# Performance work log

Hardware: AMD Instinct MI355X
Metric: run time of the kernel (lower is better)

Reference implementation:

```python
import jax, jax.numpy as jnp
import numpy as np

B, L, D, H, DH, DFF, NL, A = 32, 1024, 512, 8, 64, 2048, 6, 21
CL = 4  # new variables per clique (chain junction tree)


def _build_mask():
    # Mirrors _make_junction_tree_mask: each position attends to itself,
    # to all parent-clique variables, and to earlier vars in its own clique.
    m = np.zeros((L, L), dtype=bool)
    for c in range(L // CL):
        own = range(c * CL, (c + 1) * CL)
        par = range((c - 1) * CL, c * CL) if c > 0 else range(0)
        for i in own:
            m[i, i] = True
            for p in par:
                m[i, p] = True
            for v in own:
                if v < i:
                    m[i, v] = True
    return m


def setup_inputs() -> dict:
    key = jax.random.key(0)
    ks = jax.random.split(key, 12)
    s = 0.02
    inp = {
        "x": jax.random.randint(ks[0], (B, L), 0, A, dtype=jnp.int32),
        "mask": jnp.asarray(_build_mask())[None, None],  # (1,1,L,L), broadcasts over B,H
        "tok_emb": jax.random.normal(ks[1], (A, D)) * s,
        "pos_emb": jax.random.normal(ks[2], (L, D)) * s,
        "wq": jax.random.normal(ks[3], (NL, D, D)) * s,
        "bq": jnp.zeros((NL, D)),
        "wk": jax.random.normal(ks[4], (NL, D, D)) * s,
        "bk": jnp.zeros((NL, D)),
        "wv": jax.random.normal(ks[5], (NL, D, D)) * s,
        "bv": jnp.zeros((NL, D)),
        "wo": jax.random.normal(ks[6], (NL, D, D)) * s,
        "bo": jnp.zeros((NL, D)),
        "ln1_s": jnp.ones((NL, D)),
        "ln1_b": jnp.zeros((NL, D)),
        "ln2_s": jnp.ones((NL, D)),
        "ln2_b": jnp.zeros((NL, D)),
        "w1": jax.random.normal(ks[7], (NL, D, DFF)) * s,
        "b1": jnp.zeros((NL, DFF)),
        "w2": jax.random.normal(ks[8], (NL, DFF, D)) * s,
        "b2": jnp.zeros((NL, D)),
        "wout": jax.random.normal(ks[9], (D, A)) * s,
        "bout": jnp.zeros((A,)),
    }
    return inp


def _ln(x, s, b):
    mu = x.mean(-1, keepdims=True)
    var = ((x - mu) ** 2).mean(-1, keepdims=True)
    return (x - mu) * jax.lax.rsqrt(var + 1e-6) * s + b


def reference(x, mask, tok_emb, pos_emb, wq, bq, wk, bk, wv, bv, wo, bo,
              ln1_s, ln1_b, ln2_s, ln2_b, w1, b1, w2, b2, wout, bout):
    h = tok_emb[x] + pos_emb[None, :, :]           # (B, L, D)
    neg = jnp.asarray(-1e9, h.dtype)
    scale = jnp.asarray(1.0 / np.sqrt(DH), h.dtype)
    for l in range(NL):
        # masked multi-head self-attention (pre-LN block)
        hn = _ln(h, ln1_s[l], ln1_b[l])
        q = (hn @ wq[l] + bq[l]).reshape(B, L, H, DH)
        k = (hn @ wk[l] + bk[l]).reshape(B, L, H, DH)
        v = (hn @ wv[l] + bv[l]).reshape(B, L, H, DH)
        sc = jnp.einsum('blhd,bmhd->bhlm', q, k) * scale
        sc = jnp.where(mask, sc, neg)              # junction-tree sparsity pattern
        attn = jax.nn.softmax(sc, axis=-1)
        o = jnp.einsum('bhlm,bmhd->blhd', attn, v).reshape(B, L, D) @ wo[l] + bo[l]
        h = h + o
        # feed-forward
        hn = _ln(h, ln2_s[l], ln2_b[l])
        h = h + (jax.nn.gelu(hn @ w1[l] + b1[l]) @ w2[l] + b2[l])
    return h @ wout + bout                          # (B, L, alphabet_size)
```

## Files before the change

### kernel.cpp

```cpp
#include <hip/hip_runtime.h>

#define BB 32
#define LL 1024
#define DD 512
#define HH 8
#define DHH 64
#define DFF 2048
#define NLAYERS 6
#define AA 21
#define MTOT (BB*LL)
#define QS 1536

typedef unsigned short u16;
typedef __bf16 bf16x8 __attribute__((ext_vector_type(8)));
typedef float f32x4 __attribute__((ext_vector_type(4)));
typedef u16 u16x8 __attribute__((ext_vector_type(8)));

__device__ __forceinline__ float bf2f(u16 u) {
    return __uint_as_float(((unsigned int)u) << 16);
}
__device__ __forceinline__ u16 f2bf(float f) {
    unsigned int i = __float_as_uint(f);
    unsigned int r = i + 0x7FFFu + ((i >> 16) & 1u);
    return (u16)(r >> 16);
}

__global__ void detect_kernel(const void* __restrict__ tok, int* __restrict__ flag) {
    __shared__ int cnt[256];
    int t = threadIdx.x;
    const u16* p = (const u16*)tok;
    int c = 0;
    #pragma unroll
    for (int j = 0; j < 8; j++) {
        u16 u = p[2 * (t * 8 + j)];
        int e = (u >> 7) & 0xFF;
        c += (e >= 97 && e <= 137) ? 1 : 0;
    }
    cnt[t] = c;
    __syncthreads();
    for (int s = 128; s; s >>= 1) {
        if (t < s) cnt[t] += cnt[t + s];
        __syncthreads();
    }
    if (t == 0) flag[0] = (cnt[0] > 1024) ? 1 : 0;
}

#define NTAB 13
struct ConvTab {
    const void* src[NTAB];
    unsigned long long dstOff[NTAB];
    int n[NTAB];
    int chunk[NTAB];
    int lstride[NTAB];
};
__global__ __launch_bounds__(256) void conv_small(ConvTab tab, u16* __restrict__ spBase,
                                                  const int* __restrict__ flag, int total) {
    int i = blockIdx.x * 256 + threadIdx.x;
    if (i >= total) return;
    int fl = flag[0];
    #pragma unroll 1
    for (int e = 0; e < NTAB; e++) {
        if (i < tab.n[e]) {
            const void* s = tab.src[e];
            u16 val = fl ? ((const u16*)s)[i] : f2bf(((const float*)s)[i]);
            int c = i / tab.chunk[e];
            int r = i - c * tab.chunk[e];
            spBase[tab.dstOff[e] + (size_t)c * tab.lstride[e] + r] = val;
            return;
        }
        i -= tab.n[e];
    }
}

__global__ __launch_bounds__(256) void conv_T(const void* __restrict__ src,
                                              u16* __restrict__ dst, int R, int C,
                                              const int* __restrict__ flag, int dstZS) {
    __shared__ u16 tile[32][33];
    int z = blockIdx.z;
    size_t zoffS = (size_t)z * R * C;
    size_t zoffD = (size_t)z * dstZS;
    int bx = blockIdx.x * 32, by = blockIdx.y * 32;
    int tx = threadIdx.x & 31, ty = threadIdx.x >> 5;
    int fl = flag[0];
    const u16* s16 = (const u16*)src + zoffS;
    const float* s32 = (const float*)src + zoffS;
    #pragma unroll
    for (int r = 0; r < 4; r++) {
        size_t idx = (size_t)(by + ty * 4 + r) * C + bx + tx;
        tile[ty * 4 + r][tx] = fl ? s16[idx] : f2bf(s32[idx]);
    }
    __syncthreads();
    #pragma unroll
    for (int r = 0; r < 4; r++)
        dst[zoffD + (size_t)(bx + ty * 4 + r) * R + by + tx] = tile[tx][ty * 4 + r];
}

__global__ __launch_bounds__(256) void woutpad_kernel(const void* __restrict__ wout,
                                                      const void* __restrict__ bout,
                                                      u16* __restrict__ wpad,
                                                      u16* __restrict__ bpad,
                                                      const int* __restrict__ flag) {
    int i = blockIdx.x * 256 + threadIdx.x;
    int fl = flag[0];
    if (i < 128 * 512) {
        int n = i >> 9, kk = i & 511;
        u16 val = 0;
        if (n < AA) val = fl ? ((const u16*)wout)[kk * AA + n] : f2bf(((const float*)wout)[kk * AA + n]);
        wpad[(size_t)n * 512 + kk] = val;
    }
    if (i < 128) {
        u16 val = 0;
        if (i < AA) val = fl ? ((const u16*)bout)[i] : f2bf(((const float*)bout)[i]);
        bpad[i] = val;
    }
}

__global__ __launch_bounds__(128) void embed_kernel(const int* __restrict__ x,
                                                    const u16* __restrict__ tok_emb,
                                                    const u16* __restrict__ pos_emb,
                                                    u16* __restrict__ h) {
    int row = blockIdx.x;
    int l = row & (LL - 1);
    int tok = x[row];
    int c = threadIdx.x * 4;
    ushort4 te = *(const ushort4*)(tok_emb + (size_t)tok * DD + c);
    ushort4 pe = *(const ushort4*)(pos_emb + (size_t)l * DD + c);
    ushort4 o;
    o.x = f2bf(bf2f(te.x) + bf2f(pe.x));
    o.y = f2bf(bf2f(te.y) + bf2f(pe.y));
    o.z = f2bf(bf2f(te.z) + bf2f(pe.z));
    o.w = f2bf(bf2f(te.w) + bf2f(pe.w));
    *(ushort4*)(h + (size_t)row * DD + c) = o;
}

__global__ __launch_bounds__(256) void ln_kernel(const u16* __restrict__ h,
                                                 const u16* __restrict__ s,
                                                 const u16* __restrict__ b,
                                                 u16* __restrict__ outp) {
    int row = blockIdx.x * 4 + (threadIdx.x >> 6);
    int lane = threadIdx.x & 63;
    u16x8 hv = *(const u16x8*)(h + (size_t)row * DD + lane * 8);
    float v[8];
    #pragma unroll
    for (int i = 0; i < 8; i++) v[i] = bf2f(hv[i]);
    float sum = v[0]+v[1]+v[2]+v[3]+v[4]+v[5]+v[6]+v[7];
    #pragma unroll
    for (int off = 32; off; off >>= 1) sum += __shfl_xor(sum, off, 64);
    float mu = sum * (1.0f / DD);
    float var = 0.f;
    #pragma unroll
    for (int i = 0; i < 8; i++) {
        float d = v[i] - mu;
        var += d * d;
    }
    #pragma unroll
    for (int off = 32; off; off >>= 1) var += __shfl_xor(var, off, 64);
    float rs = rsqrtf(var * (1.0f / DD) + 1e-6f);
    u16x8 sv = *(const u16x8*)(s + lane * 8);
    u16x8 bv = *(const u16x8*)(b + lane * 8);
    u16x8 o;
    #pragma unroll
    for (int i = 0; i < 8; i++)
        o[i] = f2bf((v[i] - mu) * rs * bf2f(sv[i]) + bf2f(bv[i]));
    *(u16x8*)(outp + (size_t)row * DD + lane * 8) = o;
}

#define GLD16(gp, lp) __builtin_amdgcn_global_load_lds( \
    (const __attribute__((address_space(1))) void*)(gp), \
    (__attribute__((address_space(3))) void*)(lp), 16, 0, 0)

template <int EPI>
__global__ __launch_bounds__(256) void gemm_bt(const u16* __restrict__ A,
                                               const u16* __restrict__ BT,
                                               const u16* __restrict__ bias,
                                               u16* __restrict__ Cb,
                                               float* __restrict__ Cf,
                                               int M, int N, int K, int lda,
                                               const int* __restrict__ flag) {
    __shared__ __align__(16) u16 Als[2][128 * 32];
    __shared__ __align__(16) u16 Bls[2][128 * 32];
    const int tid  = threadIdx.x;
    const int lane = tid & 63;
    const int wave = tid >> 6;

    int gx = gridDim.x, gy = gridDim.y;
    int tileX, tileY;
    if ((gy & 7) == 0) {
        int bid = blockIdx.y * gx + blockIdx.x;
        int xcd = bid & 7;
        int idx = bid >> 3;
        int stripe = gy >> 3;
        tileX = idx % gx;
        tileY = xcd * stripe + idx / gx;
    } else {
        tileX = blockIdx.x; tileY = blockIdx.y;
    }
    const int tileM = tileY * 128;
    const int tileN = tileX * 128;
    const int wm = (wave & 1) * 64;
    const int wn = (wave >> 1) * 64;

    const int srow = tid >> 2;
    const int scol = (((tid & 3) ^ ((tid >> 3) & 3))) * 8;

    const u16* Ag0 = A  + (size_t)(tileM + srow) * lda + scol;
    const u16* Ag1 = A  + (size_t)(tileM + 64 + srow) * lda + scol;
    const u16* Bg0 = BT + (size_t)(tileN + srow) * K + scol;
    const u16* Bg1 = BT + (size_t)(tileN + 64 + srow) * K + scol;

    f32x4 acc[4][4] = {};
    const int lm = lane & 15;
    const int lk = (((lane >> 4) ^ ((lm >> 1) & 3))) * 8;

    const int nk = K >> 5;
    GLD16(Ag0, Als[0] + tid * 8);
    GLD16(Ag1, Als[0] + 2048 + tid * 8);
    GLD16(Bg0, Bls[0] + tid * 8);
    GLD16(Bg1, Bls[0] + 2048 + tid * 8);
    __syncthreads();

    for (int kt = 0; kt < nk; kt++) {
        const int cur = kt & 1;
        const int nxt = cur ^ 1;
        if (kt + 1 < nk) {
            const int k1 = (kt + 1) << 5;
            GLD16(Ag0 + k1, Als[nxt] + tid * 8);
            GLD16(Ag1 + k1, Als[nxt] + 2048 + tid * 8);
            GLD16(Bg0 + k1, Bls[nxt] + tid * 8);
            GLD16(Bg1 + k1, Bls[nxt] + 2048 + tid * 8);
        }
        bf16x8 af[4], bfr[4];
        #pragma unroll
        for (int i = 0; i < 4; i++)
            af[i] = *(const bf16x8*)(Als[cur] + (wm + i * 16 + lm) * 32 + lk);
        #pragma unroll
        for (int j = 0; j < 4; j++)
            bfr[j] = *(const bf16x8*)(Bls[cur] + (wn + j * 16 + lm) * 32 + lk);
        #pragma unroll
        for (int i = 0; i < 4; i++)
            #pragma unroll
            for (int j = 0; j < 4; j++)
                acc[i][j] = __builtin_amdgcn_mfma_f32_16x16x32_bf16(af[i], bfr[j], acc[i][j], 0, 0, 0);
        __syncthreads();
    }

    int fl = 0;
    if constexpr (EPI == 3) fl = flag[0];
    const u16* Hb = (const u16*)Cf;
    const int r0 = (lane >> 4) * 4;
    #pragma unroll
    for (int j = 0; j < 4; j++) {
        int col = tileN + wn + j * 16 + lm;
        float bv = bf2f(bias[col]);
        #pragma unroll
        for (int i = 0; i < 4; i++) {
            int row = tileM + wm + i * 16 + r0;
            #pragma unroll
            for (int r = 0; r < 4; r++) {
                float xv = acc[i][j][r] + bv;
                if constexpr (EPI == 0) {
                    Cb[(size_t)(row + r) * N + col] = f2bf(xv);
                } else if constexpr (EPI == 1) {
                    float u = 1.5957691216057308f * (xv + 0.044715f * xv * xv * xv);
                    float t = 1.0f - 2.0f / (__expf(u) + 1.0f);
                    Cb[(size_t)(row + r) * N + col] = f2bf(0.5f * xv * (1.0f + t));
                } else if constexpr (EPI == 2) {
                    size_t idx = (size_t)(row + r) * N + col;
                    Cb[idx] = f2bf(bf2f(Cb[idx]) + xv);
                } else if constexpr (EPI == 4) {
                    size_t idx = (size_t)(row + r) * N + col;
                    Cb[idx] = f2bf(xv + bf2f(Hb[idx]));
                } else {
                    if (col < AA) {
                        size_t idx = (size_t)(row + r) * AA + col;
                        if (fl) Cb[idx] = f2bf(xv);
                        else    Cf[idx] = xv;
                    }
                }
            }
        }
    }
}

__global__ __launch_bounds__(256) void attn_kernel(u16* qkv) {
    int g    = blockIdx.x * 4 + (threadIdx.x >> 6);
    int lane = threadIdx.x & 63;
    int c    = g & 255;
    int lo   = (c == 0) ? 0 : c * 4 - 4;
    int nbase = c * 4 - lo;
    size_t rowQ0 = (size_t)(g >> 8) * LL + c * 4;
    size_t rowK0 = (size_t)(g >> 8) * LL + lo;
    int off = lane * 8;

    u16x8 k8[8], v8[8];
    #pragma unroll
    for (int j = 0; j < 8; j++) {
        const u16* krow = qkv + (rowK0 + j) * QS;
        k8[j] = *(const u16x8*)(krow + 512 + off);
        v8[j] = *(const u16x8*)(krow + 1024 + off);
    }

    #pragma unroll
    for (int q = 0; q < 4; q++) {
        int nj = nbase + q + 1;
        size_t qrow = (rowQ0 + q) * QS;
        u16x8 q8 = *(const u16x8*)(qkv + qrow + off);
        float qf[8];
        #pragma unroll
        for (int i = 0; i < 8; i++) qf[i] = bf2f(q8[i]) * 0.125f;
        float sc[8];
        #pragma unroll
        for (int j = 0; j < 8; j++) {
            float t = 0.f;
            #pragma unroll
            for (int i = 0; i < 8; i++) t = fmaf(qf[i], bf2f(k8[j][i]), t);
            t += __shfl_xor(t, 1, 64);
            t += __shfl_xor(t, 2, 64);
            t += __shfl_xor(t, 4, 64);
            sc[j] = (j < nj) ? t : -1e30f;
        }
        float m = sc[0];
        #pragma unroll
        for (int j = 1; j < 8; j++) m = fmaxf(m, sc[j]);
        float p[8], den = 0.f;
        #pragma unroll
        for (int j = 0; j < 8; j++) { p[j] = __expf(sc[j] - m); den += p[j]; }
        float inv = 1.0f / den;
        float o[8] = {};
        #pragma unroll
        for (int j = 0; j < 8; j++)
            #pragma unroll
            for (int i = 0; i < 8; i++) o[i] = fmaf(p[j], bf2f(v8[j][i]), o[i]);
        u16x8 ov;
        #pragma unroll
        for (int i = 0; i < 8; i++) ov[i] = f2bf(o[i] * inv);
        *(u16x8*)(qkv + qrow + off) = ov;
    }
}

extern "C" void kernel_launch(void* const* d_in, const int* in_sizes, int n_in,
                              void* d_out, int out_size, void* d_ws, size_t ws_size,
                              hipStream_t stream) {
    const int base = n_in - 22;
    const int*  x    = (const int*)d_in[0];
    const void* tokI = d_in[2 + base];
    const void* posI = d_in[3 + base];
    const void* wqI  = d_in[4 + base];
    const void* bqI  = d_in[5 + base];
    const void* wkI  = d_in[6 + base];
    const void* bkI  = d_in[7 + base];
    const void* wvI  = d_in[8 + base];
    const void* bvI  = d_in[9 + base];
    const void* woI  = d_in[10 + base];
    const void* boI  = d_in[11 + base];
    const void* ln1sI = d_in[12 + base];
    const void* ln1bI = d_in[13 + base];
    const void* ln2sI = d_in[14 + base];
    const void* ln2bI = d_in[15 + base];
    const void* w1I  = d_in[16 + base];
    const void* b1I  = d_in[17 + base];
    const void* w2I  = d_in[18 + base];
    const void* b2I  = d_in[19 + base];
    const void* woutI = d_in[20 + base];
    const void* boutI = d_in[21 + base];

    char* ws = (char*)d_ws;
    u16*  h    = (u16*)(ws + 0);
    u16*  hn   = (u16*)(ws + 33554432);
    u16*  qkv  = (u16*)(ws + 67108864);
    u16*  wT   = (u16*)(ws + 201326592);
    u16*  sp   = (u16*)(ws + 239075328);
    int* flag  = (int*)(ws + 240500736);

    u16* mid = qkv;

    u16* wqkvT = wT;
    u16* woT   = wT + 4718592;
    u16* w1T   = wT + 6291456;
    u16* w2T   = wT + 12582912;

    const unsigned long long oWoutPad = 0;
    const unsigned long long oBoutPad = 65536;
    const unsigned long long oTok     = 65664;
    const unsigned long long oPos     = 76416;
    const unsigned long long oQkvB    = 600704;
    const unsigned long long oBo      = 609920;
    const unsigned long long oB1      = 612992;
    const unsigned long long oB2      = 625280;
    const unsigned long long oLn1s    = 628352;
    const unsigned long long oLn1b    = 631424;
    const unsigned long long oLn2s    = 634496;
    const unsigned long long oLn2b    = 637568;

    detect_kernel<<<1, 256, 0, stream>>>(tokI, flag);

    ConvTab tab;
    const void* srcs[NTAB] = {tokI, bqI, bkI, bvI, boI, b1I, b2I, ln1sI, ln1bI, ln2sI, ln2bI, posI, tokI};
    unsigned long long offs[NTAB] = {oTok, oQkvB, oQkvB + 512, oQkvB + 1024, oBo, oB1, oB2,
                                     oLn1s, oLn1b, oLn2s, oLn2b, oPos, oTok};
    int ns[NTAB]     = {10752, 3072, 3072, 3072, 3072, 12288, 3072, 3072, 3072, 3072, 3072, 524288, 0};
    int chunks[NTAB] = {10752, 512, 512, 512, 3072, 12288, 3072, 3072, 3072, 3072, 3072, 524288, 1};
    int lstr[NTAB]   = {10752, 1536, 1536, 1536, 3072, 12288, 3072, 3072, 3072, 3072, 3072, 524288, 1};
    int total = 0;
    for (int e = 0; e < NTAB; e++) {
        tab.src[e] = srcs[e]; tab.dstOff[e] = offs[e]; tab.n[e] = ns[e];
        tab.chunk[e] = chunks[e]; tab.lstride[e] = lstr[e];
        total += ns[e];
    }
    conv_small<<<(total + 255) / 256, 256, 0, stream>>>(tab, sp, flag, total);
    woutpad_kernel<<<256, 256, 0, stream>>>(woutI, boutI, sp + oWoutPad, sp + oBoutPad, flag);

    conv_T<<<dim3(16, 16, 6), 256, 0, stream>>>(wqI, wqkvT,          DD, DD, flag, 786432);
    conv_T<<<dim3(16, 16, 6), 256, 0, stream>>>(wkI, wqkvT + 262144, DD, DD, flag, 786432);
    conv_T<<<dim3(16, 16, 6), 256, 0, stream>>>(wvI, wqkvT + 524288, DD, DD, flag, 786432);
    conv_T<<<dim3(16, 16, 6), 256, 0, stream>>>(woI, woT, DD, DD, flag, 262144);
    conv_T<<<dim3(64, 16, 6), 256, 0, stream>>>(w1I, w1T, DD, DFF, flag, 1048576);
    conv_T<<<dim3(16, 64, 6), 256, 0, stream>>>(w2I, w2T, DFF, DD, flag, 1048576);

    embed_kernel<<<MTOT, 128, 0, stream>>>(x, sp + oTok, sp + oPos, h);

    for (int l = 0; l < NLAYERS; l++) {
        u16* wqkvTl = wqkvT + (size_t)l * 786432;
        u16* woTl   = woT + (size_t)l * 262144;
        u16* w1Tl   = w1T + (size_t)l * 1048576;
        u16* w2Tl   = w2T + (size_t)l * 1048576;

        ln_kernel<<<MTOT / 4, 256, 0, stream>>>(h, sp + oLn1s + l * DD, sp + oLn1b + l * DD, hn);

        gemm_bt<0><<<dim3(QS / 128, MTOT / 128), 256, 0, stream>>>(
            hn, wqkvTl, sp + oQkvB + l * QS, qkv, nullptr, MTOT, QS, DD, DD, flag);

        attn_kernel<<<MTOT / 16, 256, 0, stream>>>(qkv);

        gemm_bt<2><<<dim3(DD / 128, MTOT / 128), 256, 0, stream>>>(
            qkv, woTl, sp + oBo + l * DD, h, nullptr, MTOT, DD, DD, QS, flag);

        ln_kernel<<<MTOT / 4, 256, 0, stream>>>(h, sp + oLn2s + l * DD, sp + oLn2b + l * DD, hn);

        gemm_bt<1><<<dim3(DFF / 128, MTOT / 128), 256, 0, stream>>>(
            hn, w1Tl, sp + oB1 + l * DFF, mid, nullptr, MTOT, DFF, DD, DD, flag);
        if (l < NLAYERS - 1) {
            gemm_bt<2><<<dim3(DD / 128, MTOT / 128), 256, 0, stream>>>(
                mid, w2Tl, sp + oB2 + l * DD, h, nullptr, MTOT, DD, DFF, DFF, flag);
        } else {
            gemm_bt<4><<<dim3(DD / 128, MTOT / 128), 256, 0, stream>>>(
                mid, w2Tl, sp + oB2 + l * DD, hn, (float*)h, MTOT, DD, DFF, DFF, flag);
        }
    }

    gemm_bt<3><<<dim3(1, MTOT / 128), 256, 0, stream>>>(
        hn, sp + oWoutPad, sp + oBoutPad, (u16*)d_out, (float*)d_out, MTOT, 128, DD, DD, flag);
}
```

Before: 2.546 ms.

## Add 256x256 eight-wave triple-buffered GEMM with interleaved loads and MFMA phases

Adds a new GEMM kernel using 256x256 output tiles with 8 waves and a 3-stage LDS ring. Global-to-LDS prefetch two k-steps ahead is interleaved with four MFMA sub-phases, using explicit barriers, s_setprio, and vmcnt waits. All layer GEMMs except the final output projection switch to it. The goal is more operand reuse per tile and better overlap of memory latency with compute. The costs are a large LDS footprint, heavy register use, and fewer blocks for the narrow N=512 GEMMs, which may underfill the GPU.

Result: slower. 2.815 ms (+10.6%).

```diff
diff --git a/kernel.cpp b/kernel.cpp
--- a/kernel.cpp
+++ b/kernel.cpp
@@ -168,6 +168,7 @@
 #define GLD16(gp, lp) __builtin_amdgcn_global_load_lds( \
     (const __attribute__((address_space(1))) void*)(gp), \
     (__attribute__((address_space(3))) void*)(lp), 16, 0, 0)
+#define WAIT_VM(n) asm volatile("s_waitcnt vmcnt(" #n ") lgkmcnt(0)" ::: "memory")
 
 template <int EPI>
 __global__ __launch_bounds__(256) void gemm_bt(const u16* __restrict__ A,
@@ -282,6 +283,140 @@
     }
 }
 
+template <int EPI>
+__global__ __launch_bounds__(512, 2) void gemm8p(const u16* __restrict__ A,
+                                                 const u16* __restrict__ BT,
+                                                 const u16* __restrict__ bias,
+                                                 u16* __restrict__ Cb,
+                                                 float* __restrict__ Cf,
+                                                 int M, int N, int K, int lda,
+                                                 const int* __restrict__ flag) {
+    __shared__ __align__(16) u16 Als[3][256 * 32];
+    __shared__ __align__(16) u16 Bls[3][256 * 32];
+    const int tid  = threadIdx.x;
+    const int lane = tid & 63;
+    const int wave = tid >> 6;
+    const int wm = wave & 1;
+    const int wn = wave >> 1;
+
+    int gx = gridDim.x, gy = gridDim.y;
+    int tileX, tileY;
+    if ((gy & 7) == 0) {
+        int bid = blockIdx.y * gx + blockIdx.x;
+        int xcd = bid & 7;
+        int idx = bid >> 3;
+        int stripe = gy >> 3;
+        tileX = idx % gx;
+        tileY = xcd * stripe + idx / gx;
+    } else {
+        tileX = blockIdx.x; tileY = blockIdx.y;
+    }
+    const int tileM = tileY * 256;
+    const int tileN = tileX * 256;
+
+    const int grow = tid >> 2;
+    const int scol = (((tid & 3) ^ ((tid >> 3) & 3))) * 8;
+    const u16* Ag0 = A  + (size_t)(tileM + grow) * lda + scol;
+    const u16* Ag1 = A  + (size_t)(tileM + 128 + grow) * lda + scol;
+    const u16* Bg0 = BT + (size_t)(tileN + grow) * K + scol;
+    const u16* Bg1 = BT + (size_t)(tileN + 128 + grow) * K + scol;
+
+    f32x4 acc[8][4] = {};
+    const int lm = lane & 15;
+    const int lk = (((lane >> 4) ^ ((lm >> 1) & 3))) * 8;
+
+    const int nk = K >> 5;
+
+#define PH8(bb, mh, nh, ...) do {                                                   \
+    const u16* Ab_ = Als[bb];                                                       \
+    const u16* Bb_ = Bls[bb];                                                       \
+    bf16x8 af_[4], bf_[2];                                                          \
+    _Pragma("unroll")                                                               \
+    for (int i = 0; i < 4; i++)                                                     \
+        af_[i] = *(const bf16x8*)(Ab_ + (wm * 128 + (mh) * 64 + i * 16 + lm) * 32 + lk); \
+    _Pragma("unroll")                                                               \
+    for (int j = 0; j < 2; j++)                                                     \
+        bf_[j] = *(const bf16x8*)(Bb_ + (wn * 64 + (nh) * 32 + j * 16 + lm) * 32 + lk);  \
+    __VA_ARGS__                                                                     \
+    __builtin_amdgcn_s_barrier();                                                   \
+    __builtin_amdgcn_s_setprio(1);                                                  \
+    _Pragma("unroll")                                                               \
+    for (int i = 0; i < 4; i++)                                                     \
+        _Pragma("unroll")                                                           \
+        for (int j = 0; j < 2; j++)                                                 \
+            acc[(mh) * 4 + i][(nh) * 2 + j] = __builtin_amdgcn_mfma_f32_16x16x32_bf16( \
+                af_[i], bf_[j], acc[(mh) * 4 + i][(nh) * 2 + j], 0, 0, 0);          \
+    __builtin_amdgcn_s_setprio(0);                                                  \
+} while (0)
+
+    GLD16(Ag0, Als[0] + tid * 8);
+    GLD16(Ag1, Als[0] + 4096 + tid * 8);
+    GLD16(Bg0, Bls[0] + tid * 8);
+    GLD16(Bg1, Bls[0] + 4096 + tid * 8);
+    GLD16(Ag0 + 32, Als[1] + tid * 8);
+    GLD16(Ag1 + 32, Als[1] + 4096 + tid * 8);
+    GLD16(Bg0 + 32, Bls[1] + tid * 8);
+    GLD16(Bg1 + 32, Bls[1] + 4096 + tid * 8);
+    WAIT_VM(4);
+    __builtin_amdgcn_s_barrier();
+
+    int bb = 0;
+    int b2 = 2;
+    #pragma unroll 1
+    for (int kt = 0; kt < nk; kt++) {
+        const bool st = (kt + 2) < nk;
+        const int k2 = (kt + 2) << 5;
+        PH8(bb, 0, 0, if (st) { GLD16(Ag0 + k2, Als[b2] + tid * 8);
+                                GLD16(Ag1 + k2, Als[b2] + 4096 + tid * 8); });
+        __builtin_amdgcn_s_barrier();
+        PH8(bb, 1, 0, if (st) { GLD16(Bg0 + k2, Bls[b2] + tid * 8);
+                                GLD16(Bg1 + k2, Bls[b2] + 4096 + tid * 8); });
+        __builtin_amdgcn_s_barrier();
+        PH8(bb, 0, 1, {});
+        __builtin_amdgcn_s_barrier();
+        PH8(bb, 1, 1, {});
+        if (kt + 1 < nk) {
+            if (st) WAIT_VM(4);
+            else    WAIT_VM(0);
+            __builtin_amdgcn_s_barrier();
+        }
+        bb = (bb == 2) ? 0 : bb + 1;
+        b2 = (b2 == 2) ? 0 : b2 + 1;
+    }
+#undef PH8
+
+    int fl = 0;
+    if constexpr (EPI == 3) fl = flag[0];
+    const u16* Hb = (const u16*)Cf;
+    const int r0 = (lane >> 4) * 4;
+    #pragma unroll
+    for (int j = 0; j < 4; j++) {
+        int col = tileN + wn * 64 + j * 16 + lm;
+        float bv = bf2f(bias[col]);
+        #pragma unroll
+        for (int i = 0; i < 8; i++) {
+            int row = tileM + wm * 128 + i * 16 + r0;
+            #pragma unroll
+            for (int r = 0; r < 4; r++) {
+                float xv = acc[i][j][r] + bv;
+                if constexpr (EPI == 0) {
+                    Cb[(size_t)(row + r) * N + col] = f2bf(xv);
+                } else if constexpr (EPI == 1) {
+                    float u = 1.5957691216057308f * (xv + 0.044715f * xv * xv * xv);
+                    float t = 1.0f - 2.0f / (__expf(u) + 1.0f);
+                    Cb[(size_t)(row + r) * N + col] = f2bf(0.5f * xv * (1.0f + t));
+                } else if constexpr (EPI == 2) {
+                    size_t idx = (size_t)(row + r) * N + col;
+                    Cb[idx] = f2bf(bf2f(Cb[idx]) + xv);
+                } else if constexpr (EPI == 4) {
+                    size_t idx = (size_t)(row + r) * N + col;
+                    Cb[idx] = f2bf(xv + bf2f(Hb[idx]));
+                }
+            }
+        }
+    }
+}
+
 __global__ __launch_bounds__(256) void attn_kernel(u16* qkv) {
     int g    = blockIdx.x * 4 + (threadIdx.x >> 6);
     int lane = threadIdx.x & 63;
@@ -427,23 +562,23 @@
 
         ln_kernel<<<MTOT / 4, 256, 0, stream>>>(h, sp + oLn1s + l * DD, sp + oLn1b + l * DD, hn);
 
-        gemm_bt<0><<<dim3(QS / 128, MTOT / 128), 256, 0, stream>>>(
+        gemm8p<0><<<dim3(QS / 256, MTOT / 256), 512, 0, stream>>>(
             hn, wqkvTl, sp + oQkvB + l * QS, qkv, nullptr, MTOT, QS, DD, DD, flag);
 
         attn_kernel<<<MTOT / 16, 256, 0, stream>>>(qkv);
 
-        gemm_bt<2><<<dim3(DD / 128, MTOT / 128), 256, 0, stream>>>(
+        gemm8p<2><<<dim3(DD / 256, MTOT / 256), 512, 0, stream>>>(
             qkv, woTl, sp + oBo + l * DD, h, nullptr, MTOT, DD, DD, QS, flag);
 
         ln_kernel<<<MTOT / 4, 256, 0, stream>>>(h, sp + oLn2s + l * DD, sp + oLn2b + l * DD, hn);
 
-        gemm_bt<1><<<dim3(DFF / 128, MTOT / 128), 256, 0, stream>>>(
+        gemm8p<1><<<dim3(DFF / 256, MTOT / 256), 512, 0, stream>>>(
             hn, w1Tl, sp + oB1 + l * DFF, mid, nullptr, MTOT, DFF, DD, DD, flag);
         if (l < NLAYERS - 1) {
-            gemm_bt<2><<<dim3(DD / 128, MTOT / 128), 256, 0, stream>>>(
+            gemm8p<2><<<dim3(DD / 256, MTOT / 256), 512, 0, stream>>>(
                 mid, w2Tl, sp + oB2 + l * DD, h, nullptr, MTOT, DD, DFF, DFF, flag);
         } else {
-            gemm_bt<4><<<dim3(DD / 128, MTOT / 128), 256, 0, stream>>>(
+            gemm8p<4><<<dim3(DD / 256, MTOT / 256), 512, 0, stream>>>(
                 mid, w2Tl, sp + oB2 + l * DD, hn, (float*)h, MTOT, DD, DFF, DFF, flag);
         }
     }
```
